# Kernel tuning notes

Measured on AMD Instinct MI355X. Metric: run time of the kernel, lower is better.

The kernel has to match this reference:

```python
import jax, jax.numpy as jnp
import numpy as np

B, N, D = 4, 4096, 1024

def setup_inputs() -> dict:
    key = jax.random.key(0)
    kx, kql, kqr, kk, kv = jax.random.split(key, 5)
    std = 1.0 / D
    return {
        "x": jax.random.normal(kx, (B, N, D), dtype=jnp.float32),
        "w_query_left": jax.random.normal(kql, (D, D), dtype=jnp.float32) * std,
        "w_query_right": jax.random.normal(kqr, (D, D), dtype=jnp.float32) * std,
        "w_key": jax.random.normal(kk, (D, D), dtype=jnp.float32) * std,
        "w_value": jax.random.normal(kv, (D, D), dtype=jnp.float32) * std,
    }

def reference(x, w_query_left, w_query_right, w_key, w_value):
    # Four dxd projections
    query_left = jnp.einsum('bnd,de->bne', x, w_query_left)
    query_right = jnp.einsum('bnd,de->bne', x, w_query_right)
    key = jnp.einsum('bnd,de->bne', x, w_key)
    value = jnp.einsum('bnd,de->bne', x, w_value)
    # Elementwise gate
    query = query_left * query_right
    # Kernelized attention: key^T @ value, then query @ kv  (dropout p=0 in eval)
    kv_attn = jnp.einsum('bnd,bne->bde', key, value)   # [B, D, D]
    linear_attn = jnp.einsum('bnd,bde->bne', query, kv_attn)
    return linear_attn
```

## Files before the change

kernel.cpp:

```cpp
#include <hip/hip_runtime.h>
#include <stdint.h>

typedef short bf16x8 __attribute__((ext_vector_type(8)));
typedef float f32x4 __attribute__((ext_vector_type(4)));

__device__ __forceinline__ uint16_t f2b(float f) {
    uint32_t u = __builtin_bit_cast(uint32_t, f);
    return (uint16_t)((u + 0x7fffu + ((u >> 16) & 1u)) >> 16);
}

__device__ __forceinline__ void gll16(const void* g, void* l) {
    __builtin_amdgcn_global_load_lds(
        (const __attribute__((address_space(1))) uint32_t*)(uintptr_t)g,
        (__attribute__((address_space(3))) uint32_t*)(uint32_t)(uintptr_t)l,
        16, 0, 0);
}

__global__ __launch_bounds__(256) void cvt_tr(const float* __restrict__ x,
                                              uint16_t* __restrict__ xb,
                                              uint16_t* __restrict__ xT) {
    const int b = blockIdx.z;
    const int n0 = blockIdx.y * 64;
    const int d0 = blockIdx.x * 64;
    __shared__ uint16_t tile[64][66];
    const int t = threadIdx.x;
    const float* xbase = x + (size_t)b * 4194304;
#pragma unroll
    for (int p = 0; p < 4; p++) {
        int row = p * 16 + (t >> 4);
        int c4 = (t & 15) * 4;
        float4 v = *(const float4*)&xbase[(size_t)(n0 + row) * 1024 + d0 + c4];
        uint16_t b0 = f2b(v.x), b1 = f2b(v.y), b2 = f2b(v.z), b3 = f2b(v.w);
        tile[row][c4 + 0] = b0;
        tile[row][c4 + 1] = b1;
        tile[row][c4 + 2] = b2;
        tile[row][c4 + 3] = b3;
        uint2 pk;
        pk.x = (uint32_t)b0 | ((uint32_t)b1 << 16);
        pk.y = (uint32_t)b2 | ((uint32_t)b3 << 16);
        *(uint2*)&xb[(size_t)(b * 4096 + n0 + row) * 1024 + d0 + c4] = pk;
    }
    __syncthreads();
    uint16_t* oT = xT + (size_t)b * 4194304;
#pragma unroll
    for (int p = 0; p < 4; p++) {
        int a = p * 16 + (t >> 4);
        int b4 = (t & 15) * 4;
        uint32_t x0 = tile[b4 + 0][a], x1 = tile[b4 + 1][a];
        uint32_t x2 = tile[b4 + 2][a], x3 = tile[b4 + 3][a];
        uint2 pk;
        pk.x = x0 | (x1 << 16);
        pk.y = x2 | (x3 << 16);
        *(uint2*)&oT[(size_t)(d0 + a) * 4096 + n0 + b4] = pk;
    }
}

struct Ptr4 { const float* p[4]; };

__global__ __launch_bounds__(256) void tr_w(Ptr4 wp, uint16_t* __restrict__ out) {
    const int m = blockIdx.z;
    const float* in = wp.p[m];
    uint16_t* o = out + (size_t)m * 1048576;
    __shared__ uint16_t tile[64][68];
    int t = threadIdx.x;
    int r0 = blockIdx.y * 64, c0 = blockIdx.x * 64;
    for (int p = 0; p < 4; p++) {
        int row = p * 16 + (t >> 4);
        int c4 = (t & 15) * 4;
        float4 v = *(const float4*)&in[(size_t)(r0 + row) * 1024 + c0 + c4];
        tile[row][c4 + 0] = f2b(v.x);
        tile[row][c4 + 1] = f2b(v.y);
        tile[row][c4 + 2] = f2b(v.z);
        tile[row][c4 + 3] = f2b(v.w);
    }
    __syncthreads();
    for (int p = 0; p < 4; p++) {
        int a = p * 16 + (t >> 4);
        int b4 = (t & 15) * 4;
        uint32_t x0 = tile[b4 + 0][a], x1 = tile[b4 + 1][a];
        uint32_t x2 = tile[b4 + 2][a], x3 = tile[b4 + 3][a];
        uint2 pk;
        pk.x = x0 | (x1 << 16);
        pk.y = x2 | (x3 << 16);
        *(uint2*)&o[(size_t)(c0 + a) * 1024 + r0 + b4] = pk;
    }
}

__global__ __launch_bounds__(512, 2) void proj_gate8(const uint16_t* __restrict__ A,
                                                     const uint16_t* __restrict__ Wt,
                                                     uint16_t* __restrict__ Q) {
    __shared__ uint16_t lds[65536];
    const int t = threadIdx.x;
    const int wave = t >> 6;
    const int lane = t & 63;
    const int m0 = blockIdx.y * 256;
    const int e0 = blockIdx.x * 128;
    const uint16_t* B1 = Wt + (size_t)e0 * 1024;
    const uint16_t* B2 = Wt + 1048576 + (size_t)e0 * 1024;
    const int wm = (wave >> 1) * 64;
    const int wn = (wave & 1) * 64;

    const int srow = t >> 3;
    const int ske = ((t & 7) ^ (srow & 7)) * 8;
    const uint16_t* gA  = A  + (size_t)(m0 + srow) * 1024 + ske;
    const uint16_t* gB1 = B1 + (size_t)srow * 1024 + ske;
    const uint16_t* gB2 = B2 + (size_t)srow * 1024 + ske;

    auto STAGE = [&](int kt, int buf) {
        const int kk = kt * 64;
        uint16_t* db = lds + buf * 32768 + (wave << 9);
        gll16(gA + kk,          db);
        gll16(gA + 65536 + kk,  db + 4096);
        gll16(gA + 131072 + kk, db + 8192);
        gll16(gA + 196608 + kk, db + 12288);
        gll16(gB1 + kk,         db + 16384);
        gll16(gB1 + 65536 + kk, db + 20480);
        gll16(gB2 + kk,         db + 24576);
        gll16(gB2 + 65536 + kk, db + 28672);
    };

    const int l7x16 = (lane & 7) << 4;
    const int hi16 = (lane >> 4) << 4;
    const int es0 = (hi16 ^ l7x16) >> 1;
    const int es1 = ((64 + hi16) ^ l7x16) >> 1;
    int ar[4], br[4];
#pragma unroll
    for (int i = 0; i < 4; i++) ar[i] = (wm + i * 16 + (lane & 15)) * 64;
#pragma unroll
    for (int j = 0; j < 4; j++) br[j] = (wn + j * 16 + (lane & 15)) * 64;

    f32x4 acc1[4][4] = {};
    f32x4 acc2[4][4] = {};

    STAGE(0, 0);
    STAGE(1, 1);
    asm volatile("s_waitcnt vmcnt(8)" ::: "memory");
    __builtin_amdgcn_s_barrier();

    for (int kt = 0; kt < 16; ++kt) {
        const int buf = kt & 1;
        const uint16_t* lb = lds + buf * 32768;
        bf16x8 af[4], bq[4];

#pragma unroll
        for (int i = 0; i < 4; i++) af[i] = *(const bf16x8*)&lb[ar[i] + es0];
#pragma unroll
        for (int j = 0; j < 4; j++) bq[j] = *(const bf16x8*)&lb[16384 + br[j] + es0];
        __builtin_amdgcn_s_setprio(1);
#pragma unroll
        for (int i = 0; i < 4; i++)
#pragma unroll
            for (int j = 0; j < 4; j++)
                acc1[i][j] = __builtin_amdgcn_mfma_f32_16x16x32_bf16(af[i], bq[j],
                                                                     acc1[i][j], 0, 0, 0);
        __builtin_amdgcn_s_setprio(0);

#pragma unroll
        for (int j = 0; j < 4; j++) bq[j] = *(const bf16x8*)&lb[24576 + br[j] + es0];
        __builtin_amdgcn_s_setprio(1);
#pragma unroll
        for (int i = 0; i < 4; i++)
#pragma unroll
            for (int j = 0; j < 4; j++)
                acc2[i][j] = __builtin_amdgcn_mfma_f32_16x16x32_bf16(af[i], bq[j],
                                                                     acc2[i][j], 0, 0, 0);
        __builtin_amdgcn_s_setprio(0);

#pragma unroll
        for (int i = 0; i < 4; i++) af[i] = *(const bf16x8*)&lb[ar[i] + es1];
#pragma unroll
        for (int j = 0; j < 4; j++) bq[j] = *(const bf16x8*)&lb[16384 + br[j] + es1];
        __builtin_amdgcn_s_setprio(1);
#pragma unroll
        for (int i = 0; i < 4; i++)
#pragma unroll
            for (int j = 0; j < 4; j++)
                acc1[i][j] = __builtin_amdgcn_mfma_f32_16x16x32_bf16(af[i], bq[j],
                                                                     acc1[i][j], 0, 0, 0);
        __builtin_amdgcn_s_setprio(0);

#pragma unroll
        for (int j = 0; j < 4; j++) bq[j] = *(const bf16x8*)&lb[24576 + br[j] + es1];
        __builtin_amdgcn_s_setprio(1);
#pragma unroll
        for (int i = 0; i < 4; i++)
#pragma unroll
            for (int j = 0; j < 4; j++)
                acc2[i][j] = __builtin_amdgcn_mfma_f32_16x16x32_bf16(af[i], bq[j],
                                                                     acc2[i][j], 0, 0, 0);
        __builtin_amdgcn_s_setprio(0);

        asm volatile("s_waitcnt lgkmcnt(0)" ::: "memory");
        __builtin_amdgcn_sched_barrier(0);
        __builtin_amdgcn_s_barrier();
        if (kt < 14) {
            STAGE(kt + 2, buf);
            asm volatile("s_waitcnt vmcnt(8)" ::: "memory");
        } else {
            asm volatile("s_waitcnt vmcnt(0)" ::: "memory");
        }
        __builtin_amdgcn_s_barrier();
    }

    const int rl = (lane >> 4) * 4;
    const int cl = lane & 15;
#pragma unroll
    for (int i = 0; i < 4; i++)
#pragma unroll
        for (int j = 0; j < 4; j++)
#pragma unroll
            for (int r = 0; r < 4; r++) {
                float g = acc1[i][j][r] * acc2[i][j][r];
                Q[(size_t)(m0 + wm + i * 16 + rl + r) * 1024 + e0 + wn + j * 16 + cl] = f2b(g);
            }
}

__global__ __launch_bounds__(256) void gemm_kv_splitk(const uint16_t* __restrict__ VT,
                                                      const uint16_t* __restrict__ KT,
                                                      float* __restrict__ P) {
    const int z = blockIdx.z;
    const int batch = z >> 1, ks = z & 1;
    const uint16_t* Ab = VT + (size_t)batch * 4194304 + ks * 2048;
    const uint16_t* Bb = KT + (size_t)batch * 4194304 + ks * 2048;

    __shared__ uint16_t lA[4096];
    __shared__ uint16_t lB[4096];

    const int t = threadIdx.x;
    const int wave = t >> 6;
    const int lane = t & 63;
    const int m0 = blockIdx.y * 128;
    const int n0 = blockIdx.x * 128;
    const int wm = (wave >> 1) * 64;
    const int wn = (wave & 1) * 64;

    const uint16_t* gA0 = Ab + (size_t)(m0 + (t >> 2)) * 4096 + (t & 3) * 8;
    const uint16_t* gB0 = Bb + (size_t)(n0 + (t >> 2)) * 4096 + (t & 3) * 8;
    uint16_t* lA0 = lA + wave * 512;
    uint16_t* lA1 = lA + 2048 + wave * 512;
    uint16_t* lB0 = lB + wave * 512;
    uint16_t* lB1 = lB + 2048 + wave * 512;

    f32x4 acc[4][4] = {};

    const int arow = wm + (lane & 15);
    const int brow = wn + (lane & 15);
    const int koff = (lane >> 4) * 8;

    for (int k0 = 0; k0 < 2048; k0 += 32) {
        __syncthreads();
        gll16(gA0 + k0, lA0);
        gll16(gA0 + (size_t)64 * 4096 + k0, lA1);
        gll16(gB0 + k0, lB0);
        gll16(gB0 + (size_t)64 * 4096 + k0, lB1);
        __syncthreads();

        bf16x8 af[4], bfr[4];
#pragma unroll
        for (int i = 0; i < 4; i++)
            af[i] = *(const bf16x8*)&lA[(arow + i * 16) * 32 + koff];
#pragma unroll
        for (int i = 0; i < 4; i++)
            bfr[i] = *(const bf16x8*)&lB[(brow + i * 16) * 32 + koff];
#pragma unroll
        for (int i = 0; i < 4; i++)
#pragma unroll
            for (int j = 0; j < 4; j++)
                acc[i][j] = __builtin_amdgcn_mfma_f32_16x16x32_bf16(af[i], bfr[j],
                                                                    acc[i][j], 0, 0, 0);
    }

    float* Pb = P + (size_t)z * 1048576;
    const int crow = m0 + wm + (lane >> 4) * 4;
    const int ccol = n0 + wn + (lane & 15);
#pragma unroll
    for (int i = 0; i < 4; i++)
#pragma unroll
        for (int j = 0; j < 4; j++)
#pragma unroll
            for (int r = 0; r < 4; r++)
                Pb[(size_t)(crow + i * 16 + r) * 1024 + ccol + j * 16] = acc[i][j][r];
}

__global__ __launch_bounds__(256) void reduce_kv(const float4* __restrict__ P,
                                                 uint2* __restrict__ G) {
    int i = blockIdx.x * 256 + threadIdx.x;
    int b = i >> 18;
    int r = i & 262143;
    const float4* base = P + (size_t)b * 524288 + r;
    float4 s0 = base[0];
    float4 s1 = base[262144];
    float x = s0.x + s1.x;
    float y = s0.y + s1.y;
    float zz = s0.z + s1.z;
    float w = s0.w + s1.w;
    uint2 o;
    o.x = (uint32_t)f2b(x) | ((uint32_t)f2b(y) << 16);
    o.y = (uint32_t)f2b(zz) | ((uint32_t)f2b(w) << 16);
    G[i] = o;
}

__global__ __launch_bounds__(256) void gemm_nt_bf16(const uint16_t* __restrict__ A,
                                                    int lda, int az,
                                                    const uint16_t* __restrict__ Bt,
                                                    int ldb,
                                                    uint16_t* __restrict__ C,
                                                    int ldc, int cz) {
    const uint16_t* Ab = A + (size_t)blockIdx.z * az;
    uint16_t* Cb = C + (size_t)blockIdx.z * cz;

    __shared__ uint16_t lA[4096];
    __shared__ uint16_t lB[4096];

    const int t = threadIdx.x;
    const int wave = t >> 6;
    const int lane = t & 63;
    const int m0 = blockIdx.y * 128;
    const int n0 = blockIdx.x * 128;
    const int wm = (wave >> 1) * 64;
    const int wn = (wave & 1) * 64;

    const uint16_t* gA0 = Ab + (size_t)(m0 + (t >> 2)) * lda + (t & 3) * 8;
    const uint16_t* gB0 = Bt + (size_t)(n0 + (t >> 2)) * ldb + (t & 3) * 8;
    uint16_t* lA0 = lA + wave * 512;
    uint16_t* lA1 = lA + 2048 + wave * 512;
    uint16_t* lB0 = lB + wave * 512;
    uint16_t* lB1 = lB + 2048 + wave * 512;

    f32x4 acc[4][4] = {};

    const int arow = wm + (lane & 15);
    const int brow = wn + (lane & 15);
    const int koff = (lane >> 4) * 8;

    for (int k0 = 0; k0 < 1024; k0 += 32) {
        __syncthreads();
        gll16(gA0 + k0, lA0);
        gll16(gA0 + (size_t)64 * lda + k0, lA1);
        gll16(gB0 + k0, lB0);
        gll16(gB0 + (size_t)64 * ldb + k0, lB1);
        __syncthreads();

        bf16x8 af[4], bfr[4];
#pragma unroll
        for (int i = 0; i < 4; i++)
            af[i] = *(const bf16x8*)&lA[(arow + i * 16) * 32 + koff];
#pragma unroll
        for (int i = 0; i < 4; i++)
            bfr[i] = *(const bf16x8*)&lB[(brow + i * 16) * 32 + koff];
#pragma unroll
        for (int i = 0; i < 4; i++)
#pragma unroll
            for (int j = 0; j < 4; j++)
                acc[i][j] = __builtin_amdgcn_mfma_f32_16x16x32_bf16(af[i], bfr[j],
                                                                    acc[i][j], 0, 0, 0);
    }

    const int crow = m0 + wm + (lane >> 4) * 4;
    const int ccol = n0 + wn + (lane & 15);
#pragma unroll
    for (int i = 0; i < 4; i++)
#pragma unroll
        for (int j = 0; j < 4; j++)
#pragma unroll
            for (int r = 0; r < 4; r++)
                Cb[(size_t)(crow + i * 16 + r) * ldc + ccol + j * 16] = f2b(acc[i][j][r]);
}

__global__ __launch_bounds__(256) void gemm_out(const uint16_t* __restrict__ A,
                                                const uint16_t* __restrict__ Bt,
                                                float* __restrict__ C) {
    const uint16_t* Ab = A + (size_t)blockIdx.z * 4194304;
    const uint16_t* Bb = Bt + (size_t)blockIdx.z * 1048576;

    __shared__ uint16_t lA[4096];
    __shared__ uint16_t lB[4096];

    const int t = threadIdx.x;
    const int wave = t >> 6;
    const int lane = t & 63;
    const int m0 = blockIdx.y * 128;
    const int n0 = blockIdx.x * 128;
    const int wm = (wave >> 1) * 64;
    const int wn = (wave & 1) * 64;

    const uint16_t* gA0 = Ab + (size_t)(m0 + (t >> 2)) * 1024 + (t & 3) * 8;
    const uint16_t* gB0 = Bb + (size_t)(n0 + (t >> 2)) * 1024 + (t & 3) * 8;
    uint16_t* lA0 = lA + wave * 512;
    uint16_t* lA1 = lA + 2048 + wave * 512;
    uint16_t* lB0 = lB + wave * 512;
    uint16_t* lB1 = lB + 2048 + wave * 512;

    f32x4 acc[4][4] = {};

    const int arow = wm + (lane & 15);
    const int brow = wn + (lane & 15);
    const int koff = (lane >> 4) * 8;

    for (int k0 = 0; k0 < 1024; k0 += 32) {
        __syncthreads();
        gll16(gA0 + k0, lA0);
        gll16(gA0 + (size_t)64 * 1024 + k0, lA1);
        gll16(gB0 + k0, lB0);
        gll16(gB0 + (size_t)64 * 1024 + k0, lB1);
        __syncthreads();

        bf16x8 af[4], bfr[4];
#pragma unroll
        for (int i = 0; i < 4; i++)
            af[i] = *(const bf16x8*)&lA[(arow + i * 16) * 32 + koff];
#pragma unroll
        for (int i = 0; i < 4; i++)
            bfr[i] = *(const bf16x8*)&lB[(brow + i * 16) * 32 + koff];
#pragma unroll
        for (int i = 0; i < 4; i++)
#pragma unroll
            for (int j = 0; j < 4; j++)
                acc[i][j] = __builtin_amdgcn_mfma_f32_16x16x32_bf16(af[i], bfr[j],
                                                                    acc[i][j], 0, 0, 0);
    }

    float* Cb = C + (size_t)blockIdx.z * 4194304;
    const int crow = m0 + wm + (lane >> 4) * 4;
    const int ccol = n0 + wn + (lane & 15);
#pragma unroll
    for (int i = 0; i < 4; i++)
#pragma unroll
        for (int j = 0; j < 4; j++)
#pragma unroll
            for (int r = 0; r < 4; r++)
                Cb[(size_t)(crow + i * 16 + r) * 1024 + ccol + j * 16] = acc[i][j][r];
}

extern "C" void kernel_launch(void* const* d_in, const int* in_sizes, int n_in,
                              void* d_out, int out_size, void* d_ws, size_t ws_size,
                              hipStream_t stream) {
    const float* x = (const float*)d_in[0];

    uint16_t* ws  = (uint16_t*)d_ws;
    uint16_t* xb  = ws;
    uint16_t* xT  = ws + 16777216;
    uint16_t* Wt  = ws + 33554432;
    uint16_t* Q   = ws + 37748736;
    float*    P   = (float*)(ws + 54525952);
    uint16_t* G   = ws + 71303168;
    uint16_t* H   = ws + 75497472;
    uint16_t* kvT = ws + 79691776;

    cvt_tr<<<dim3(16, 64, 4), 256, 0, stream>>>(x, xb, xT);

    Ptr4 wp;
    wp.p[0] = (const float*)d_in[1];
    wp.p[1] = (const float*)d_in[2];
    wp.p[2] = (const float*)d_in[3];
    wp.p[3] = (const float*)d_in[4];
    tr_w<<<dim3(16, 16, 4), 256, 0, stream>>>(wp, Wt);

    proj_gate8<<<dim3(8, 64), 512, 0, stream>>>(xb, Wt, Q);

    gemm_kv_splitk<<<dim3(8, 8, 8), 256, 0, stream>>>(xT, xT, P);

    reduce_kv<<<4096, 256, 0, stream>>>((const float4*)P, (uint2*)G);

    gemm_nt_bf16<<<dim3(32, 8, 1), 256, 0, stream>>>(Wt + 3 * 1048576, 1024, 0,
                                                     G, 1024, H, 4096, 0);

    gemm_nt_bf16<<<dim3(8, 8, 4), 256, 0, stream>>>(H, 4096, 1024,
                                                    Wt + 2 * 1048576, 1024,
                                                    kvT, 1024, 1048576);

    gemm_out<<<dim3(8, 32, 4), 256, 0, stream>>>(Q, kvT, (float*)d_out);
}
```

Before: 372.6 us.

## Restructure gated projection GEMM into four half-K LDS stages with finer barriers

The gated projection kernel now splits each 64-wide K tile into two 32-wide halves held in four rotating LDS slots, with a new XOR swizzle layout for A and both weight tiles. Loads for the next tile are issued per half, right after the slot that was just consumed, instead of once per full tile. Barriers and waits are interleaved with the MFMA groups in a ping-pong style so that memory traffic overlaps compute more evenly. The many extra workgroup barriers per iteration could add synchronization stalls.

Result: slower. 389.8 us (+4.6%).

```diff
diff --git a/kernel.cpp b/kernel.cpp
--- a/kernel.cpp
+++ b/kernel.cpp
@@ -100,52 +100,61 @@
     const int wm = (wave >> 1) * 64;
     const int wn = (wave & 1) * 64;
 
-    const int srow = t >> 3;
-    const int ske = ((t & 7) ^ (srow & 7)) * 8;
-    const uint16_t* gA  = A  + (size_t)(m0 + srow) * 1024 + ske;
-    const uint16_t* gB1 = B1 + (size_t)srow * 1024 + ske;
-    const uint16_t* gB2 = B2 + (size_t)srow * 1024 + ske;
-
-    auto STAGE = [&](int kt, int buf) {
-        const int kk = kt * 64;
-        uint16_t* db = lds + buf * 32768 + (wave << 9);
-        gll16(gA + kk,          db);
-        gll16(gA + 65536 + kk,  db + 4096);
-        gll16(gA + 131072 + kk, db + 8192);
-        gll16(gA + 196608 + kk, db + 12288);
-        gll16(gB1 + kk,         db + 16384);
-        gll16(gB1 + 65536 + kk, db + 20480);
-        gll16(gB2 + kk,         db + 24576);
-        gll16(gB2 + 65536 + kk, db + 28672);
+    int LsA0 = t * 16;
+    int LsA1 = 8192 + t * 16;
+    int LsB  = t * 16;
+    int gbA0 = LsA0 ^ (((LsA0 >> 7) & 7) << 4);
+    int gbA1 = LsA1 ^ (((LsA1 >> 7) & 7) << 4);
+    int gbB  = LsB  ^ (((LsB  >> 7) & 7) << 4);
+    const uint16_t* srcA0 = A + (size_t)(m0 + (gbA0 >> 6)) * 1024 + ((gbA0 & 63) >> 1);
+    const uint16_t* srcA1 = A + (size_t)(m0 + (gbA1 >> 6)) * 1024 + ((gbA1 & 63) >> 1);
+    const uint16_t* srcB1 = B1 + (size_t)(gbB >> 6) * 1024 + ((gbB & 63) >> 1);
+    const uint16_t* srcB2 = B2 + (size_t)(gbB >> 6) * 1024 + ((gbB & 63) >> 1);
+
+    auto STAGE = [&](int kt_, int ks_) {
+        const int h = (2 * kt_ + ks_) & 3;
+        const int kb = kt_ * 64 + ks_ * 32;
+        uint16_t* db = lds + h * 16384 + (wave << 9);
+        gll16(srcA0 + kb, db);
+        gll16(srcA1 + kb, db + 4096);
+        gll16(srcB1 + kb, db + 8192);
+        gll16(srcB2 + kb, db + 12288);
     };
 
-    const int l7x16 = (lane & 7) << 4;
-    const int hi16 = (lane >> 4) << 4;
-    const int es0 = (hi16 ^ l7x16) >> 1;
-    const int es1 = ((64 + hi16) ^ l7x16) >> 1;
-    int ar[4], br[4];
-#pragma unroll
-    for (int i = 0; i < 4; i++) ar[i] = (wm + i * 16 + (lane & 15)) * 64;
-#pragma unroll
-    for (int j = 0; j < 4; j++) br[j] = (wn + j * 16 + (lane & 15)) * 64;
+    const int cb = (lane >> 4) << 4;
+    int aoff[4], b1off[4], b2off[4];
+#pragma unroll
+    for (int i = 0; i < 4; i++) {
+        int g = (wm + i * 16 + (lane & 15)) * 64 + cb;
+        aoff[i] = (g ^ (((g >> 7) & 7) << 4)) >> 1;
+    }
+#pragma unroll
+    for (int j = 0; j < 4; j++) {
+        int g = (wn + j * 16 + (lane & 15)) * 64 + cb;
+        int sw = (g ^ (((g >> 7) & 7) << 4)) >> 1;
+        b1off[j] = 8192 + sw;
+        b2off[j] = 12288 + sw;
+    }
 
     f32x4 acc1[4][4] = {};
     f32x4 acc2[4][4] = {};
 
-    STAGE(0, 0);
-    STAGE(1, 1);
-    asm volatile("s_waitcnt vmcnt(8)" ::: "memory");
+    STAGE(0, 0); STAGE(0, 1); STAGE(1, 0); STAGE(1, 1);
+    asm volatile("s_waitcnt vmcnt(12)" ::: "memory");
     __builtin_amdgcn_s_barrier();
 
     for (int kt = 0; kt < 16; ++kt) {
-        const int buf = kt & 1;
-        const uint16_t* lb = lds + buf * 32768;
+        const uint16_t* lb0 = lds + ((2 * kt) & 3) * 16384;
+        const uint16_t* lb1 = lds + ((2 * kt + 1) & 3) * 16384;
         bf16x8 af[4], bq[4];
 
 #pragma unroll
-        for (int i = 0; i < 4; i++) af[i] = *(const bf16x8*)&lb[ar[i] + es0];
-#pragma unroll
-        for (int j = 0; j < 4; j++) bq[j] = *(const bf16x8*)&lb[16384 + br[j] + es0];
+        for (int i = 0; i < 4; i++) af[i] = *(const bf16x8*)&lb0[aoff[i]];
+#pragma unroll
+        for (int j = 0; j < 4; j++) bq[j] = *(const bf16x8*)&lb0[b1off[j]];
+        __builtin_amdgcn_s_barrier();
+        asm volatile("s_waitcnt lgkmcnt(0)" ::: "memory");
+        __builtin_amdgcn_sched_barrier(0);
         __builtin_amdgcn_s_setprio(1);
 #pragma unroll
         for (int i = 0; i < 4; i++)
@@ -154,9 +163,13 @@
                 acc1[i][j] = __builtin_amdgcn_mfma_f32_16x16x32_bf16(af[i], bq[j],
                                                                      acc1[i][j], 0, 0, 0);
         __builtin_amdgcn_s_setprio(0);
-
-#pragma unroll
-        for (int j = 0; j < 4; j++) bq[j] = *(const bf16x8*)&lb[24576 + br[j] + es0];
+        __builtin_amdgcn_s_barrier();
+
+#pragma unroll
+        for (int j = 0; j < 4; j++) bq[j] = *(const bf16x8*)&lb0[b2off[j]];
+        __builtin_amdgcn_s_barrier();
+        asm volatile("s_waitcnt lgkmcnt(0)" ::: "memory");
+        __builtin_amdgcn_sched_barrier(0);
         __builtin_amdgcn_s_setprio(1);
 #pragma unroll
         for (int i = 0; i < 4; i++)
@@ -165,11 +178,18 @@
                 acc2[i][j] = __builtin_amdgcn_mfma_f32_16x16x32_bf16(af[i], bq[j],
                                                                      acc2[i][j], 0, 0, 0);
         __builtin_amdgcn_s_setprio(0);
-
-#pragma unroll
-        for (int i = 0; i < 4; i++) af[i] = *(const bf16x8*)&lb[ar[i] + es1];
-#pragma unroll
-        for (int j = 0; j < 4; j++) bq[j] = *(const bf16x8*)&lb[16384 + br[j] + es1];
+        if (kt < 15) { asm volatile("s_waitcnt vmcnt(8)" ::: "memory"); }
+        else         { asm volatile("s_waitcnt vmcnt(0)" ::: "memory"); }
+        __builtin_amdgcn_s_barrier();
+        if (kt < 14) STAGE(kt + 2, 0);
+
+#pragma unroll
+        for (int i = 0; i < 4; i++) af[i] = *(const bf16x8*)&lb1[aoff[i]];
+#pragma unroll
+        for (int j = 0; j < 4; j++) bq[j] = *(const bf16x8*)&lb1[b1off[j]];
+        __builtin_amdgcn_s_barrier();
+        asm volatile("s_waitcnt lgkmcnt(0)" ::: "memory");
+        __builtin_amdgcn_sched_barrier(0);
         __builtin_amdgcn_s_setprio(1);
 #pragma unroll
         for (int i = 0; i < 4; i++)
@@ -178,9 +198,13 @@
                 acc1[i][j] = __builtin_amdgcn_mfma_f32_16x16x32_bf16(af[i], bq[j],
                                                                      acc1[i][j], 0, 0, 0);
         __builtin_amdgcn_s_setprio(0);
-
-#pragma unroll
-        for (int j = 0; j < 4; j++) bq[j] = *(const bf16x8*)&lb[24576 + br[j] + es1];
+        __builtin_amdgcn_s_barrier();
+
+#pragma unroll
+        for (int j = 0; j < 4; j++) bq[j] = *(const bf16x8*)&lb1[b2off[j]];
+        __builtin_amdgcn_s_barrier();
+        asm volatile("s_waitcnt lgkmcnt(0)" ::: "memory");
+        __builtin_amdgcn_sched_barrier(0);
         __builtin_amdgcn_s_setprio(1);
 #pragma unroll
         for (int i = 0; i < 4; i++)
@@ -189,17 +213,11 @@
                 acc2[i][j] = __builtin_amdgcn_mfma_f32_16x16x32_bf16(af[i], bq[j],
                                                                      acc2[i][j], 0, 0, 0);
         __builtin_amdgcn_s_setprio(0);
-
-        asm volatile("s_waitcnt lgkmcnt(0)" ::: "memory");
-        __builtin_amdgcn_sched_barrier(0);
-        __builtin_amdgcn_s_barrier();
-        if (kt < 14) {
-            STAGE(kt + 2, buf);
-            asm volatile("s_waitcnt vmcnt(8)" ::: "memory");
-        } else {
-            asm volatile("s_waitcnt vmcnt(0)" ::: "memory");
-        }
-        __builtin_amdgcn_s_barrier();
+        if (kt < 14)       { asm volatile("s_waitcnt vmcnt(8)" ::: "memory"); }
+        else if (kt == 14) { asm volatile("s_waitcnt vmcnt(4)" ::: "memory"); }
+        else               { asm volatile("s_waitcnt vmcnt(0)" ::: "memory"); }
+        __builtin_amdgcn_s_barrier();
+        if (kt < 14) STAGE(kt + 2, 1);
     }
 
     const int rl = (lane >> 4) * 4;
```
